# Kernel tuning notes

Hardware: AMD Instinct MI355X
Metric: run time of the kernel (lower is better)

Reference implementation:

```python
import jax, jax.numpy as jnp
import numpy as np

N_NODES = 100000
N_EDGES = 1600000
IN_DIM = 128
HID_DIM = 32
OUT_DIM = 64
N_REL = 8
N_CLASSES = 2


def setup_inputs() -> dict:
    key = jax.random.key(0)
    ks = jax.random.split(key, 12)
    x = jax.random.normal(ks[0], (N_NODES, IN_DIM), dtype=jnp.float32)
    edge_index = jax.random.randint(ks[1], (2, N_EDGES), 0, N_NODES, dtype=jnp.int64)
    edge_type = jax.random.randint(ks[2], (N_EDGES,), 0, N_REL, dtype=jnp.int64)
    # FastRGCNConv params: per-relation weight W [R, in, out], root weight, bias
    def glorot(k, shape):
        fan_in, fan_out = shape[-2], shape[-1]
        s = jnp.sqrt(6.0 / (fan_in + fan_out))
        return jax.random.uniform(k, shape, jnp.float32, -s, s)
    W1 = glorot(ks[3], (N_REL, IN_DIM, HID_DIM))
    root1 = glorot(ks[4], (IN_DIM, HID_DIM))
    b1 = jnp.zeros((HID_DIM,), jnp.float32)
    W2 = glorot(ks[5], (N_REL, HID_DIM, OUT_DIM))
    root2 = glorot(ks[6], (HID_DIM, OUT_DIM))
    b2 = jnp.zeros((OUT_DIM,), jnp.float32)
    lin_w = glorot(ks[7], (OUT_DIM, N_CLASSES))
    lin_b = jnp.zeros((N_CLASSES,), jnp.float32)
    return {"x": x, "edge_index": edge_index, "edge_type": edge_type,
            "W1": W1, "root1": root1, "b1": b1,
            "W2": W2, "root2": root2, "b2": b2,
            "lin_w": lin_w, "lin_b": lin_b}


def _fast_rgcn_conv(x, W, root, b, src, dst, etype, n_nodes):
    """FastRGCNConv: per-relation transform, gather by (src, relation),
    mean-aggregate by destination, plus root transform and bias."""
    # Transform all nodes by all relation weights: [N, R, H]
    xW = jnp.einsum('nf,rfh->nrh', x, W)
    # Per-edge message: relation-specific transformed source feature [E, H]
    msg = xW[src, etype]
    agg = jax.ops.segment_sum(msg, dst, num_segments=n_nodes)
    deg = jax.ops.segment_sum(jnp.ones((src.shape[0],), x.dtype), dst,
                              num_segments=n_nodes)
    agg = agg / jnp.maximum(deg, 1.0)[:, None]  # mean aggregation
    return agg + x @ root + b


def reference(x, edge_index, edge_type, W1, root1, b1, W2, root2, b2, lin_w, lin_b):
    src, dst = edge_index[0], edge_index[1]
    n = x.shape[0]
    h = jax.nn.relu(_fast_rgcn_conv(x, W1, root1, b1, src, dst, edge_type, n))
    h = _fast_rgcn_conv(h, W2, root2, b2, src, dst, edge_type, n)
    return h @ lin_w + lin_b
```

## Files before the change

### kernel.cpp

```cpp
#include <hip/hip_runtime.h>

#define NN      100000
#define IN_DIM  128
#define HID     32
#define ODIM    64
#define L1C     288
#define L2K     288
#define NWGS    196
#define NCB     784
#define CCAP    40
#define RECCAP  2304
#define G2ST    296

using bf16x8 = __attribute__((ext_vector_type(8))) short;
using f32x4  = __attribute__((ext_vector_type(4))) float;

__device__ __forceinline__ float bf2f(short s) {
    unsigned int u = ((unsigned int)(unsigned short)s) << 16;
    float f; __builtin_memcpy(&f, &u, 4); return f;
}
__device__ __forceinline__ short f2bf(float f) {
    unsigned int u; __builtin_memcpy(&u, &f, 4);
    u += 0x7fffu + ((u >> 16) & 1u);
    return (short)(u >> 16);
}
__device__ __forceinline__ float ldf(const void* p, int i, int f32) {
    return f32 ? ((const float*)p)[i] : bf2f(((const short*)p)[i]);
}
__device__ __forceinline__ int ldi(const int* p, long long i, int i64) {
    return i64 ? p[2 * i] : p[(int)i];
}

__global__ __launch_bounds__(1024) void detect(const short* __restrict__ x,
                                               const short* __restrict__ W1,
                                               const short* __restrict__ r1,
                                               const short* __restrict__ W2,
                                               const short* __restrict__ r2,
                                               const short* __restrict__ lw,
                                               const int* __restrict__ ei,
                                               const int* __restrict__ et,
                                               int* __restrict__ flags) {
    __shared__ int cnt[8];
    if (threadIdx.x < 8) cnt[threadIdx.x] = 0;
    __syncthreads();
    const short* ptrs[6] = {x, W1, r1, W2, r2, lw};
    const int    nsmp[6] = {1024, 1024, 1024, 1024, 1024, 64};
    int t = threadIdx.x;
#pragma unroll
    for (int j = 0; j < 6; ++j) {
        if (t < nsmp[j]) {
            unsigned int s = (unsigned short)ptrs[j][2 * t];
            unsigned int e = (s >> 7) & 0xFF;
            if (e >= 140u || (e >= 1u && e <= 100u)) atomicAdd(&cnt[j], 1);
        }
    }
    if (t < 128) {
        if (ei[2 * t + 1] != 0) atomicAdd(&cnt[6], 1);
        if (et[2 * t + 1] != 0) atomicAdd(&cnt[7], 1);
    }
    __syncthreads();
    if (t == 0) {
        const int ns[6] = {1024, 1024, 1024, 1024, 1024, 64};
        for (int j = 0; j < 6; ++j) flags[j] = (cnt[j] * 4 > ns[j]) ? 1 : 0;
        flags[6] = (cnt[6] == 0) ? 1 : 0;
        flags[7] = (cnt[7] == 0) ? 1 : 0;
    }
}

__global__ __launch_bounds__(256) void prep_all(const void* __restrict__ W1,
                                                const void* __restrict__ root1,
                                                const void* __restrict__ W2,
                                                const void* __restrict__ root2,
                                                const short* __restrict__ b1,
                                                const short* __restrict__ b2,
                                                const void* __restrict__ lin_w,
                                                const short* __restrict__ lin_b,
                                                short* __restrict__ w1t,
                                                short* __restrict__ w2ct,
                                                short* __restrict__ smallc,
                                                const int* __restrict__ flags) {
    int gi = blockIdx.x * 256 + threadIdx.x;
    if (gi < L1C * IN_DIM) {
        int c = gi >> 7, f = gi & 127;
        float v;
        if (c < 256) { int r = c >> 5, h = c & 31; v = ldf(W1, (r * IN_DIM + f) * HID + h, flags[1]); }
        else         { v = ldf(root1, f * HID + (c - 256), flags[2]); }
        w1t[c * IN_DIM + f] = f2bf(v);
        return;
    }
    int i2 = gi - L1C * IN_DIM;
    if (i2 < ODIM * L2K) {
        int c = i2 / L2K, k = i2 % L2K;
        float v;
        if (k < 256) { int r = k >> 5, kk = k & 31; v = ldf(W2, (r * HID + kk) * ODIM + c, flags[3]); }
        else         { v = ldf(root2, (k - 256) * ODIM + c, flags[4]); }
        w2ct[c * L2K + k] = f2bf(v);
        return;
    }
    int i3 = i2 - ODIM * L2K;
    if (i3 < 256) {
        if (i3 < 32)        smallc[i3] = b1[i3];
        else if (i3 < 96)   smallc[i3] = b2[i3 - 32];
        else if (i3 < 224)  smallc[i3] = f2bf(ldf(lin_w, i3 - 96, flags[5]));
        else if (i3 < 226)  smallc[i3] = lin_b[i3 - 224];
    }
}

__global__ __launch_bounds__(1024) void scatter_coarse(const int* __restrict__ ei,
                                                       const int* __restrict__ et,
                                                       int* __restrict__ cnt,
                                                       int* __restrict__ seg, int E,
                                                       const int* __restrict__ flags) {
    __shared__ int cur[NCB];
    if (threadIdx.x < NCB) cur[threadIdx.x] = 0;
    __syncthreads();
    int i64 = flags[6], t64 = flags[7];
    int epw = (E + NWGS - 1) / NWGS;
    int lo = blockIdx.x * epw;
    int hi = lo + epw; if (hi > E) hi = E;
    for (int i = lo + threadIdx.x; i < hi; i += 1024) {
        int s = ldi(ei, i, i64);
        int d = ldi(ei, (long long)E + i, i64);
        int r = ldi(et, i, t64);
        int cb = d >> 7;
        int pos = atomicAdd(&cur[cb], 1);
        if (pos < CCAP)
            seg[(cb * NWGS + (int)blockIdx.x) * CCAP + pos] = ((d & 127) << 20) | (s << 3) | r;
    }
    __syncthreads();
    if (threadIdx.x < NCB) {
        int c = cur[threadIdx.x];
        cnt[blockIdx.x * NCB + threadIdx.x] = c < CCAP ? c : CCAP;
    }
}

__global__ __launch_bounds__(64) void cb_sum(const int* __restrict__ cnt,
                                             int* __restrict__ cbTot) {
    int cb = blockIdx.x, lane = threadIdx.x;
    int t = 0;
    for (int g = lane; g < NWGS; g += 64) t += cnt[g * NCB + cb];
#pragma unroll
    for (int o = 32; o > 0; o >>= 1) t += __shfl_down(t, o, 64);
    if (lane == 0) cbTot[cb] = t;
}

__global__ __launch_bounds__(256) void build_cb(const int* __restrict__ cnt,
                                                const int* __restrict__ seg,
                                                const int* __restrict__ cbTot,
                                                int* __restrict__ off,
                                                float* __restrict__ inv_deg,
                                                int* __restrict__ packed) {
    __shared__ int cntl[NWGS], soff[NWGS];
    __shared__ int recs[RECCAP];
    __shared__ int deg8[1024], base8[1024], kcur8[1024];
    __shared__ int stmp[256];
    __shared__ int gbase_s;
    int cb = blockIdx.x, tid = threadIdx.x;
    {
        int part = 0;
        for (int j = tid; j < cb; j += 256) part += cbTot[j];
        stmp[tid] = part; __syncthreads();
        for (int o = 128; o > 0; o >>= 1) {
            if (tid < o) stmp[tid] += stmp[tid + o];
            __syncthreads();
        }
        if (tid == 0) gbase_s = stmp[0];
        __syncthreads();
    }
    if (tid < NWGS) cntl[tid] = cnt[tid * NCB + cb];
#pragma unroll
    for (int j = 0; j < 4; ++j) { deg8[tid + j * 256] = 0; kcur8[tid + j * 256] = 0; }
    __syncthreads();
    int v = (tid < NWGS) ? cntl[tid] : 0;
    stmp[tid] = v; __syncthreads();
    for (int o = 1; o < 256; o <<= 1) {
        int u = (tid >= o) ? stmp[tid - o] : 0;
        __syncthreads();
        stmp[tid] += u;
        __syncthreads();
    }
    if (tid < NWGS) soff[tid] = stmp[tid] - v;
    int tot = stmp[255]; if (tot > RECCAP) tot = RECCAP;
    __syncthreads();
    int wave = tid >> 6, lane = tid & 63;
    for (int g = wave; g < NWGS; g += 4) {
        int c = cntl[g], b = soff[g];
        const int* sp = seg + (cb * NWGS + g) * CCAP;
        for (int e = lane; e < c; e += 64)
            if (b + e < RECCAP) recs[b + e] = sp[e];
    }
    __syncthreads();
    for (int i = tid; i < tot; i += 256) {
        int rec = recs[i];
        atomicAdd(&deg8[((rec >> 20) << 3) | (rec & 7)], 1);
    }
    __syncthreads();
    int k0 = tid * 4;
    int d0 = deg8[k0], d1 = deg8[k0 + 1], d2 = deg8[k0 + 2], d3 = deg8[k0 + 3];
    int s01 = d0 + d1, sum4 = s01 + d2 + d3;
    stmp[tid] = sum4; __syncthreads();
    for (int o = 1; o < 256; o <<= 1) {
        int u = (tid >= o) ? stmp[tid - o] : 0;
        __syncthreads();
        stmp[tid] += u;
        __syncthreads();
    }
    int excl = stmp[tid] - sum4;
    base8[k0] = excl; base8[k0 + 1] = excl + d0;
    base8[k0 + 2] = excl + s01; base8[k0 + 3] = excl + s01 + d2;
    __syncthreads();
    int gbase = gbase_s;
    if (tid < 128) {
        int b0 = base8[tid * 8];
        int b1 = (tid < 127) ? base8[(tid + 1) * 8] : tot;
        int dv = b1 - b0;
        int node = cb * 128 + tid;
        if (node <= NN) {
            off[node] = gbase + b0;
            if (node < NN) inv_deg[node] = 1.0f / (float)(dv > 1 ? dv : 1);
        }
    }
    __syncthreads();
    for (int i = tid; i < tot; i += 256) {
        int rec = recs[i];
        int key = ((rec >> 20) << 3) | (rec & 7);
        int p = atomicAdd(&kcur8[key], 1);
        packed[gbase + base8[key] + p] = (((rec >> 20) & 15) << 24) | (rec & 0xFFFFF);
    }
}

__global__ __launch_bounds__(256) void gemm1(const void* __restrict__ x,
                                             const short* __restrict__ w1t,
                                             short* __restrict__ xw,
                                             const int* __restrict__ flags) {
    int wave = threadIdx.x >> 6, lane = threadIdx.x & 63;
    int m = lane & 15, quad = lane >> 4;
    int row0 = (blockIdx.x * 4 + wave) * 64;
    if (row0 >= NN) return;

    bf16x8 a[4][4];
    int fp32 = flags[0];
#pragma unroll
    for (int t = 0; t < 4; ++t) {
        int row = row0 + t * 16 + m;
        int rc = row < NN ? row : NN - 1;
        if (fp32) {
            const float* xr = (const float*)x + rc * IN_DIM + quad * 8;
#pragma unroll
            for (int kt = 0; kt < 4; ++kt) {
                const f32x4* q = (const f32x4*)(xr + kt * 32);
                f32x4 u0 = q[0], u1 = q[1];
                bf16x8 tt;
                tt[0] = f2bf(u0[0]); tt[1] = f2bf(u0[1]); tt[2] = f2bf(u0[2]); tt[3] = f2bf(u0[3]);
                tt[4] = f2bf(u1[0]); tt[5] = f2bf(u1[1]); tt[6] = f2bf(u1[2]); tt[7] = f2bf(u1[3]);
                a[t][kt] = tt;
            }
        } else {
            const short* xr = (const short*)x + rc * IN_DIM + quad * 8;
#pragma unroll
            for (int kt = 0; kt < 4; ++kt) a[t][kt] = *(const bf16x8*)(xr + kt * 32);
        }
    }

    for (int ct = 0; ct < 18; ++ct) {
        const short* wp = w1t + (ct * 16 + m) * IN_DIM + quad * 8;
        bf16x8 b[4];
#pragma unroll
        for (int kt = 0; kt < 4; ++kt) b[kt] = *(const bf16x8*)(wp + kt * 32);
#pragma unroll
        for (int t = 0; t < 4; ++t) {
            f32x4 acc = {0.f, 0.f, 0.f, 0.f};
#pragma unroll
            for (int kt = 0; kt < 4; ++kt)
                acc = __builtin_amdgcn_mfma_f32_16x16x32_bf16(a[t][kt], b[kt], acc, 0, 0, 0);
#pragma unroll
            for (int i = 0; i < 4; ++i) {
                int r = row0 + t * 16 + quad * 4 + i;
                if (r < NN) xw[r * L1C + ct * 16 + m] = f2bf(acc[i]);
            }
        }
    }
}

__global__ __launch_bounds__(256) void agg1(const short* __restrict__ xw,
                                            const int* __restrict__ off,
                                            const int* __restrict__ packed,
                                            const float* __restrict__ inv_deg,
                                            const short* __restrict__ smallc,
                                            short* __restrict__ h) {
    int lane = threadIdx.x & 31;
    int node = blockIdx.x * 8 + (threadIdx.x >> 5);
    if (node >= NN) return;
    int s = off[node], e = off[node + 1];
    float acc = 0.f;
    int i = s;
    for (; i + 7 < e; i += 8) {
        int pk0 = packed[i],     pk1 = packed[i + 1], pk2 = packed[i + 2], pk3 = packed[i + 3];
        int pk4 = packed[i + 4], pk5 = packed[i + 5], pk6 = packed[i + 6], pk7 = packed[i + 7];
        float v0 = bf2f(xw[((pk0 >> 3) & 0x1FFFF) * L1C + (pk0 & 7) * 32 + lane]);
        float v1 = bf2f(xw[((pk1 >> 3) & 0x1FFFF) * L1C + (pk1 & 7) * 32 + lane]);
        float v2 = bf2f(xw[((pk2 >> 3) & 0x1FFFF) * L1C + (pk2 & 7) * 32 + lane]);
        float v3 = bf2f(xw[((pk3 >> 3) & 0x1FFFF) * L1C + (pk3 & 7) * 32 + lane]);
        float v4 = bf2f(xw[((pk4 >> 3) & 0x1FFFF) * L1C + (pk4 & 7) * 32 + lane]);
        float v5 = bf2f(xw[((pk5 >> 3) & 0x1FFFF) * L1C + (pk5 & 7) * 32 + lane]);
        float v6 = bf2f(xw[((pk6 >> 3) & 0x1FFFF) * L1C + (pk6 & 7) * 32 + lane]);
        float v7 = bf2f(xw[((pk7 >> 3) & 0x1FFFF) * L1C + (pk7 & 7) * 32 + lane]);
        acc += ((v0 + v1) + (v2 + v3)) + ((v4 + v5) + (v6 + v7));
    }
    for (; i + 3 < e; i += 4) {
        int pk0 = packed[i], pk1 = packed[i + 1], pk2 = packed[i + 2], pk3 = packed[i + 3];
        float v0 = bf2f(xw[((pk0 >> 3) & 0x1FFFF) * L1C + (pk0 & 7) * 32 + lane]);
        float v1 = bf2f(xw[((pk1 >> 3) & 0x1FFFF) * L1C + (pk1 & 7) * 32 + lane]);
        float v2 = bf2f(xw[((pk2 >> 3) & 0x1FFFF) * L1C + (pk2 & 7) * 32 + lane]);
        float v3 = bf2f(xw[((pk3 >> 3) & 0x1FFFF) * L1C + (pk3 & 7) * 32 + lane]);
        acc += (v0 + v1) + (v2 + v3);
    }
    for (; i < e; ++i) {
        int pk = packed[i];
        acc += bf2f(xw[((pk >> 3) & 0x1FFFF) * L1C + (pk & 7) * 32 + lane]);
    }
    float v = acc * inv_deg[node] + bf2f(xw[node * L1C + 256 + lane]) + bf2f(smallc[lane]);
    h[node * HID + lane] = f2bf(v > 0.f ? v : 0.f);
}

__global__ __launch_bounds__(256) void agg2_fused(const short* __restrict__ h,
                                                  const int* __restrict__ off,
                                                  const int* __restrict__ packed,
                                                  const float* __restrict__ inv_deg,
                                                  const short* __restrict__ w2ct,
                                                  const short* __restrict__ smallc,
                                                  float* __restrict__ out) {
    __shared__ __align__(16) short g2l[16 * G2ST];
    __shared__ float red[4][16][2];
    __shared__ float invl[16];
    int tid = threadIdx.x;
    int row0 = blockIdx.x * 16;
    if (tid < 16) invl[tid] = inv_deg[row0 + tid];
    {
        unsigned* gz = (unsigned*)g2l;
        const int nu = 16 * G2ST / 2;
        for (int j = tid; j < nu; j += 256) gz[j] = 0;
    }
    __syncthreads();

    int node = tid >> 4, l = tid & 15;
    int st = off[row0 + node], en = off[row0 + node + 1];
    float inv = invl[node];
    const short* hp = h + l * 2;
    short* grow = g2l + node * G2ST + l * 2;
    float a0 = 0.f, a1 = 0.f;
    int cur = -1;

    auto acc_edge = [&](int pk, unsigned hv) {
        int rel = pk & 7;
        if (rel != cur) {
            if (cur >= 0) {
                unsigned w = ((unsigned)(unsigned short)f2bf(a1 * inv) << 16)
                           | (unsigned short)f2bf(a0 * inv);
                *(unsigned*)(grow + cur * 32) = w;
            }
            a0 = 0.f; a1 = 0.f; cur = rel;
        }
        a0 += bf2f((short)(hv & 0xFFFF));
        a1 += bf2f((short)(hv >> 16));
    };

    int i = st;
    for (; i + 3 < en; i += 4) {
        int p0 = packed[i], p1 = packed[i + 1], p2 = packed[i + 2], p3 = packed[i + 3];
        unsigned v0 = *(const unsigned*)(hp + ((p0 >> 3) & 0x1FFFF) * HID);
        unsigned v1 = *(const unsigned*)(hp + ((p1 >> 3) & 0x1FFFF) * HID);
        unsigned v2 = *(const unsigned*)(hp + ((p2 >> 3) & 0x1FFFF) * HID);
        unsigned v3 = *(const unsigned*)(hp + ((p3 >> 3) & 0x1FFFF) * HID);
        acc_edge(p0, v0); acc_edge(p1, v1); acc_edge(p2, v2); acc_edge(p3, v3);
    }
    for (; i < en; ++i) {
        int p = packed[i];
        unsigned v = *(const unsigned*)(hp + ((p >> 3) & 0x1FFFF) * HID);
        acc_edge(p, v);
    }
    if (cur >= 0) {
        unsigned w = ((unsigned)(unsigned short)f2bf(a1 * inv) << 16)
                   | (unsigned short)f2bf(a0 * inv);
        *(unsigned*)(grow + cur * 32) = w;
    }
    *(unsigned*)(grow + 256) = *(const unsigned*)(h + (row0 + node) * HID + l * 2);
    __syncthreads();

    int wave = tid >> 6, lane = tid & 63;
    int m15 = lane & 15, quad = lane >> 4;
    const short* wp = w2ct + (wave * 16 + m15) * L2K + quad * 8;
    bf16x8 a[9], b[9];
#pragma unroll
    for (int kt = 0; kt < 9; ++kt) {
        b[kt] = *(const bf16x8*)(wp + kt * 32);
        a[kt] = *(const bf16x8*)(&g2l[m15 * G2ST + quad * 8 + kt * 32]);
    }
    f32x4 acc = {0.f, 0.f, 0.f, 0.f};
#pragma unroll
    for (int kt = 0; kt < 9; ++kt)
        acc = __builtin_amdgcn_mfma_f32_16x16x32_bf16(a[kt], b[kt], acc, 0, 0, 0);

    int c = wave * 16 + m15;
    float lw0 = bf2f(smallc[96 + c * 2 + 0]);
    float lw1 = bf2f(smallc[96 + c * 2 + 1]);
    float b2c = bf2f(smallc[32 + c]);
    float pr0[4], pr1[4];
#pragma unroll
    for (int i2 = 0; i2 < 4; ++i2) {
        float v = acc[i2] + b2c;
        pr0[i2] = v * lw0;
        pr1[i2] = v * lw1;
    }
#pragma unroll
    for (int o = 1; o < 16; o <<= 1) {
#pragma unroll
        for (int i2 = 0; i2 < 4; ++i2) {
            pr0[i2] += __shfl_xor(pr0[i2], o, 64);
            pr1[i2] += __shfl_xor(pr1[i2], o, 64);
        }
    }
    if (m15 == 0) {
#pragma unroll
        for (int i2 = 0; i2 < 4; ++i2) {
            red[wave][quad * 4 + i2][0] = pr0[i2];
            red[wave][quad * 4 + i2][1] = pr1[i2];
        }
    }
    __syncthreads();
    if (tid < 32) {
        int row = tid >> 1, j = tid & 1;
        float v = red[0][row][j] + red[1][row][j] + red[2][row][j] + red[3][row][j]
                + bf2f(smallc[224 + j]);
        out[(row0 + row) * 2 + j] = v;
    }
}

extern "C" void kernel_launch(void* const* d_in, const int* in_sizes, int n_in,
                              void* d_out, int out_size, void* d_ws, size_t ws_size,
                              hipStream_t stream) {
    const void* x     = d_in[0];
    const int*  ei    = (const int*)d_in[1];
    const int*  etype = (const int*)d_in[2];
    const void* W1    = d_in[3];
    const void* root1 = d_in[4];
    const void* b1    = d_in[5];
    const void* W2    = d_in[6];
    const void* root2 = d_in[7];
    const void* b2    = d_in[8];
    const void* lin_w = d_in[9];
    const void* lin_b = d_in[10];
    float* out = (float*)d_out;

    const int E = in_sizes[2];

    char* p = (char*)d_ws;
    auto alloc = [&](size_t bytes) { char* r = p; p += (bytes + 255) & ~(size_t)255; return (void*)r; };
    int*   flags   = (int*)  alloc(256);
    int*   off     = (int*)  alloc((size_t)(NN + 1) * 4);
    float* inv_deg = (float*)alloc((size_t)NN * 4);
    int*   packed  = (int*)  alloc((size_t)E * 4);
    int*   cnt     = (int*)  alloc((size_t)NWGS * NCB * 4);
    int*   cbTot   = (int*)  alloc((size_t)NCB * 4);
    int*   seg     = (int*)  alloc((size_t)NCB * NWGS * CCAP * 4);
    short* w1t     = (short*)alloc((size_t)L1C * IN_DIM * 2);
    short* w2ct    = (short*)alloc((size_t)ODIM * L2K * 2);
    short* smallc  = (short*)alloc(256 * 2);
    short* h       = (short*)alloc((size_t)NN * HID * 2);
    short* xw1     = (short*)alloc((size_t)NN * L1C * 2);

    detect<<<1, 1024, 0, stream>>>((const short*)x, (const short*)W1, (const short*)root1,
                                   (const short*)W2, (const short*)root2, (const short*)lin_w,
                                   ei, etype, flags);
    const int prep_items = L1C * IN_DIM + ODIM * L2K + 256;
    prep_all<<<(prep_items + 255) / 256, 256, 0, stream>>>(W1, root1, W2, root2,
                                                           (const short*)b1, (const short*)b2,
                                                           lin_w, (const short*)lin_b,
                                                           w1t, w2ct, smallc, flags);

    scatter_coarse<<<NWGS, 1024, 0, stream>>>(ei, etype, cnt, seg, E, flags);
    cb_sum<<<NCB, 64, 0, stream>>>(cnt, cbTot);
    build_cb<<<NCB, 256, 0, stream>>>(cnt, seg, cbTot, off, inv_deg, packed);

    gemm1<<<((NN + 63) / 64 + 3) / 4, 256, 0, stream>>>(x, w1t, xw1, flags);
    agg1<<<(NN + 7) / 8, 256, 0, stream>>>(xw1, off, packed, inv_deg, smallc, h);
    agg2_fused<<<NN / 16, 256, 0, stream>>>(h, off, packed, inv_deg, w2ct, smallc, out);
}
```

Baseline: 288.8 us.

## Use per-(node,relation) offsets and LDS-staged edge lists in layer-2 aggregation

build_cb now also writes per-(node,relation) CSR offsets (off8). agg2_fused uses them to loop over the 8 relations directly instead of detecting relation changes per edge, and stages each block's packed edge records in shared memory first. The LDS zeroing of g2l is dropped because every relation slot is now written explicitly. This removes per-edge branching and redundant global loads of packed indices, at the cost of an extra offsets array write and a fallback path when a block has more than 512 edges.

Result: slower. 302.4 us (+4.7%).

```diff
diff --git a/kernel.cpp b/kernel.cpp
--- a/kernel.cpp
+++ b/kernel.cpp
@@ -11,6 +11,7 @@
 #define CCAP    40
 #define RECCAP  2304
 #define G2ST    296
+#define PKCAP   512
 
 using bf16x8 = __attribute__((ext_vector_type(8))) short;
 using f32x4  = __attribute__((ext_vector_type(4))) float;
@@ -148,6 +149,7 @@
                                                 const int* __restrict__ seg,
                                                 const int* __restrict__ cbTot,
                                                 int* __restrict__ off,
+                                                int* __restrict__ off8,
                                                 float* __restrict__ inv_deg,
                                                 int* __restrict__ packed) {
     __shared__ int cntl[NWGS], soff[NWGS];
@@ -220,6 +222,8 @@
             if (node < NN) inv_deg[node] = 1.0f / (float)(dv > 1 ? dv : 1);
         }
     }
+    for (int j = tid; j < 1024; j += 256) off8[cb * 1024 + j] = gbase + base8[j];
+    if (cb == NCB - 1 && tid == 0) off8[NCB * 1024] = gbase + tot;
     __syncthreads();
     for (int i = tid; i < tot; i += 256) {
         int rec = recs[i];
@@ -324,66 +328,62 @@
 }
 
 __global__ __launch_bounds__(256) void agg2_fused(const short* __restrict__ h,
-                                                  const int* __restrict__ off,
+                                                  const int* __restrict__ off8,
                                                   const int* __restrict__ packed,
                                                   const float* __restrict__ inv_deg,
                                                   const short* __restrict__ w2ct,
                                                   const short* __restrict__ smallc,
                                                   float* __restrict__ out) {
     __shared__ __align__(16) short g2l[16 * G2ST];
+    __shared__ int pk_l[PKCAP];
+    __shared__ int bnd[129];
     __shared__ float red[4][16][2];
     __shared__ float invl[16];
     int tid = threadIdx.x;
     int row0 = blockIdx.x * 16;
+    if (tid < 129) bnd[tid] = off8[row0 * 8 + tid];
     if (tid < 16) invl[tid] = inv_deg[row0 + tid];
-    {
-        unsigned* gz = (unsigned*)g2l;
-        const int nu = 16 * G2ST / 2;
-        for (int j = tid; j < nu; j += 256) gz[j] = 0;
-    }
+    int st = off8[row0 * 8];
+    int tot = off8[row0 * 8 + 128] - st;
+    for (int j = tid; j < tot && j < PKCAP; j += 256) pk_l[j] = packed[st + j];
     __syncthreads();
 
     int node = tid >> 4, l = tid & 15;
-    int st = off[row0 + node], en = off[row0 + node + 1];
-    float inv = invl[node];
     const short* hp = h + l * 2;
     short* grow = g2l + node * G2ST + l * 2;
-    float a0 = 0.f, a1 = 0.f;
-    int cur = -1;
-
-    auto acc_edge = [&](int pk, unsigned hv) {
-        int rel = pk & 7;
-        if (rel != cur) {
-            if (cur >= 0) {
-                unsigned w = ((unsigned)(unsigned short)f2bf(a1 * inv) << 16)
-                           | (unsigned short)f2bf(a0 * inv);
-                *(unsigned*)(grow + cur * 32) = w;
+    float inv = invl[node];
+
+    auto do_node = [&](auto LD) {
+        for (int r = 0; r < 8; ++r) {
+            int s = bnd[node * 8 + r] - st;
+            int en = bnd[node * 8 + r + 1] - st;
+            float a0 = 0.f, a1 = 0.f;
+            int i = s;
+            for (; i + 3 < en; i += 4) {
+                int p0 = LD(i), p1 = LD(i + 1), p2 = LD(i + 2), p3 = LD(i + 3);
+                unsigned v0 = *(const unsigned*)(hp + ((p0 >> 3) & 0x1FFFF) * HID);
+                unsigned v1 = *(const unsigned*)(hp + ((p1 >> 3) & 0x1FFFF) * HID);
+                unsigned v2 = *(const unsigned*)(hp + ((p2 >> 3) & 0x1FFFF) * HID);
+                unsigned v3 = *(const unsigned*)(hp + ((p3 >> 3) & 0x1FFFF) * HID);
+                a0 += (bf2f((short)(v0 & 0xFFFF)) + bf2f((short)(v1 & 0xFFFF)))
+                    + (bf2f((short)(v2 & 0xFFFF)) + bf2f((short)(v3 & 0xFFFF)));
+                a1 += (bf2f((short)(v0 >> 16)) + bf2f((short)(v1 >> 16)))
+                    + (bf2f((short)(v2 >> 16)) + bf2f((short)(v3 >> 16)));
             }
-            a0 = 0.f; a1 = 0.f; cur = rel;
-        }
-        a0 += bf2f((short)(hv & 0xFFFF));
-        a1 += bf2f((short)(hv >> 16));
+            for (; i < en; ++i) {
+                int p = LD(i);
+                unsigned v = *(const unsigned*)(hp + ((p >> 3) & 0x1FFFF) * HID);
+                a0 += bf2f((short)(v & 0xFFFF));
+                a1 += bf2f((short)(v >> 16));
+            }
+            unsigned w = ((unsigned)(unsigned short)f2bf(a1 * inv) << 16)
+                       | (unsigned short)f2bf(a0 * inv);
+            *(unsigned*)(grow + r * 32) = w;
+        }
     };
-
-    int i = st;
-    for (; i + 3 < en; i += 4) {
-        int p0 = packed[i], p1 = packed[i + 1], p2 = packed[i + 2], p3 = packed[i + 3];
-        unsigned v0 = *(const unsigned*)(hp + ((p0 >> 3) & 0x1FFFF) * HID);
-        unsigned v1 = *(const unsigned*)(hp + ((p1 >> 3) & 0x1FFFF) * HID);
-        unsigned v2 = *(const unsigned*)(hp + ((p2 >> 3) & 0x1FFFF) * HID);
-        unsigned v3 = *(const unsigned*)(hp + ((p3 >> 3) & 0x1FFFF) * HID);
-        acc_edge(p0, v0); acc_edge(p1, v1); acc_edge(p2, v2); acc_edge(p3, v3);
-    }
-    for (; i < en; ++i) {
-        int p = packed[i];
-        unsigned v = *(const unsigned*)(hp + ((p >> 3) & 0x1FFFF) * HID);
-        acc_edge(p, v);
-    }
-    if (cur >= 0) {
-        unsigned w = ((unsigned)(unsigned short)f2bf(a1 * inv) << 16)
-                   | (unsigned short)f2bf(a0 * inv);
-        *(unsigned*)(grow + cur * 32) = w;
-    }
+    if (tot <= PKCAP) do_node([&](int j) { return pk_l[j]; });
+    else              do_node([&](int j) { return (j < PKCAP) ? pk_l[j] : packed[st + j]; });
+
     *(unsigned*)(grow + 256) = *(const unsigned*)(h + (row0 + node) * HID + l * 2);
     __syncthreads();
 
@@ -458,6 +458,7 @@
     auto alloc = [&](size_t bytes) { char* r = p; p += (bytes + 255) & ~(size_t)255; return (void*)r; };
     int*   flags   = (int*)  alloc(256);
     int*   off     = (int*)  alloc((size_t)(NN + 1) * 4);
+    int*   off8    = (int*)  alloc((size_t)(NCB * 1024 + 1) * 4);
     float* inv_deg = (float*)alloc((size_t)NN * 4);
     int*   packed  = (int*)  alloc((size_t)E * 4);
     int*   cnt     = (int*)  alloc((size_t)NWGS * NCB * 4);
@@ -480,9 +481,9 @@
 
     scatter_coarse<<<NWGS, 1024, 0, stream>>>(ei, etype, cnt, seg, E, flags);
     cb_sum<<<NCB, 64, 0, stream>>>(cnt, cbTot);
-    build_cb<<<NCB, 256, 0, stream>>>(cnt, seg, cbTot, off, inv_deg, packed);
+    build_cb<<<NCB, 256, 0, stream>>>(cnt, seg, cbTot, off, off8, inv_deg, packed);
 
     gemm1<<<((NN + 63) / 64 + 3) / 4, 256, 0, stream>>>(x, w1t, xw1, flags);
     agg1<<<(NN + 7) / 8, 256, 0, stream>>>(xw1, off, packed, inv_deg, smallc, h);
-    agg2_fused<<<NN / 16, 256, 0, stream>>>(h, off, packed, inv_deg, w2ct, smallc, out);
-}
+    agg2_fused<<<NN / 16, 256, 0, stream>>>(h, off8, packed, inv_deg, w2ct, smallc, out);
+}
```
